# Optimization experiments

Measured on AMD Instinct MI355X. Metric: run time of the kernel, lower is better.

Reference implementation:

```python
import jax, jax.numpy as jnp
import numpy as np

B, T, C, H, HD = 4, 2048, 1024, 16, 64

def setup_inputs() -> dict:
    key = jax.random.key(0)
    ks = jax.random.split(key, 9)
    s = 1.0 / np.sqrt(C)
    return {
        "x":  jax.random.normal(ks[0], (B, T, C), jnp.float32),
        "Wq": jax.random.normal(ks[1], (H, C, HD), jnp.float32) * s,
        "bq": jax.random.normal(ks[2], (H, HD), jnp.float32) * 0.02,
        "Wk": jax.random.normal(ks[3], (H, C, HD), jnp.float32) * s,
        "bk": jax.random.normal(ks[4], (H, HD), jnp.float32) * 0.02,
        "Wv": jax.random.normal(ks[5], (H, C, HD), jnp.float32) * s,
        "bv": jax.random.normal(ks[6], (H, HD), jnp.float32) * 0.02,
        "Wo": jax.random.normal(ks[7], (C, C), jnp.float32) * s,
        "bo": jax.random.normal(ks[8], (C,), jnp.float32) * 0.02,
    }

def reference(x, Wq, bq, Wk, bk, Wv, bv, Wo, bo):
    # Batched per-head linear projections: [B,T,C] x [H,C,D] -> [B,H,T,D]
    q = jnp.einsum('btc,hcd->bhtd', x, Wq) + bq[None, :, None, :]
    k = jnp.einsum('btc,hcd->bhtd', x, Wk) + bk[None, :, None, :]
    v = jnp.einsum('btc,hcd->bhtd', x, Wv) + bv[None, :, None, :]
    scale = 1.0 / jnp.sqrt(jnp.asarray(HD, q.dtype))
    scores = jnp.einsum('bhtd,bhsd->bhts', q, k) * scale  # [B,H,T,T]
    causal = jnp.tril(jnp.ones((T, T), dtype=bool))
    scores = jnp.where(causal[None, None, :, :], scores, -jnp.inf)
    attn = jax.nn.softmax(scores, axis=-1)
    out = jnp.einsum('bhts,bhsd->bhtd', attn, v)          # [B,H,T,D]
    concat = out.transpose(0, 2, 1, 3).reshape(B, T, C)   # concat heads
    return concat @ Wo + bo
```

## Files before the change

### kernel.cpp

```cpp
#include <hip/hip_runtime.h>
#include <stdint.h>

#define TSEQ 2048
#define NHEAD 16

typedef __attribute__((ext_vector_type(8))) short bf16x8;
typedef __attribute__((ext_vector_type(4))) short bf16x4;
typedef __attribute__((ext_vector_type(4))) float f32x4;

__device__ __forceinline__ unsigned short f2bf(float f) {
  union { float f; uint32_t u; } c;
  c.f = f;
  uint32_t u = c.u;
  u += 0x7fffu + ((u >> 16) & 1u);
  return (unsigned short)(u >> 16);
}

__device__ __forceinline__ float fexp2(float x) {
#if __has_builtin(__builtin_amdgcn_exp2f)
  return __builtin_amdgcn_exp2f(x);
#else
  return __builtin_exp2f(x);
#endif
}

using as3_void  = __attribute__((address_space(3))) void;
using as1_cvoid = const __attribute__((address_space(1))) void;

__device__ __forceinline__ void gld_lds16(const void* g, void* l) {
  __builtin_amdgcn_global_load_lds((as1_cvoid*)g, (as3_void*)l, 16, 0, 0);
}


__global__ void prep_all(const float* __restrict__ x,
                         const float* __restrict__ Wq, const float* __restrict__ Wk,
                         const float* __restrict__ Wv, const float* __restrict__ Wo,
                         unsigned short* __restrict__ xb, unsigned short* __restrict__ BT,
                         unsigned short* __restrict__ WoT) {
  __shared__ unsigned short tile[64][72];
  const int bidx = blockIdx.x;
  const int t = threadIdx.x;
  if (bidx < 8192) {
    const int i = bidx * 256 + t;
    float4 v = ((const float4*)x)[i];
    int e = i * 4;
    int m = e >> 10, k = e & 1023;
    int ks = k ^ ((m & 7) << 3);
    ushort4 o;
    o.x = f2bf(v.x); o.y = f2bf(v.y); o.z = f2bf(v.z); o.w = f2bf(v.w);
    *(ushort4*)(xb + (size_t)m * 1024 + ks) = o;
  } else if (bidx < 8960) {
    const int bb = bidx - 8192;
    const int c0 = (bb & 15) * 64, h = (bb >> 4) & 15, z = bb >> 8;
    const float* W = (z == 0) ? Wq : (z == 1) ? Wk : Wv;
    const float* src = W + ((size_t)h * 1024 + c0) * 64;
#pragma unroll
    for (int p = 0; p < 16; ++p) {
      int idx = p * 256 + t;
      int cc = idx >> 6, d = idx & 63;
      tile[cc][d] = f2bf(src[(size_t)cc * 64 + d]);
    }
    __syncthreads();
    unsigned short* dst = BT + ((size_t)z * 1024 + (size_t)h * 64) * 1024 + c0;
#pragma unroll
    for (int p = 0; p < 16; ++p) {
      int idx = p * 256 + t;
      int d = idx >> 6, cc = idx & 63;
      dst[(size_t)d * 1024 + (cc ^ ((d & 7) << 3))] = tile[cc][d];
    }
  } else {
    const int bb = bidx - 8960;
    const int k0 = (bb & 15) * 64, n0 = (bb >> 4) * 64;
#pragma unroll
    for (int p = 0; p < 16; ++p) {
      int idx = p * 256 + t;
      int kk = idx >> 6, nn = idx & 63;
      tile[kk][nn] = f2bf(Wo[(size_t)(k0 + kk) * 1024 + n0 + nn]);
    }
    __syncthreads();
#pragma unroll
    for (int p = 0; p < 16; ++p) {
      int idx = p * 256 + t;
      int nn = idx >> 6, kk = idx & 63;
      WoT[(size_t)(n0 + nn) * 1024 + k0 + (kk ^ ((nn & 7) << 3))] = tile[kk][nn];
    }
  }
}


template <int MODE>
__global__ __launch_bounds__(256) void gemm_bt(
    const unsigned short* __restrict__ A, const unsigned short* __restrict__ BTm,
    const float* __restrict__ bias0, const float* __restrict__ bias1,
    const float* __restrict__ bias2,
    unsigned short* __restrict__ qo, unsigned short* __restrict__ ko,
    unsigned short* __restrict__ vto, float* __restrict__ outf,
    int K, int N) {
  __shared__ __align__(16) char lds[65536];

  const int tid = threadIdx.x, lane = tid & 63, wv = tid >> 6;
  const int wr = wv >> 1, wc = wv & 1;
  const int g = lane >> 4, r = lane & 15;
  const int m0 = blockIdx.x * 128, n0 = blockIdx.y * 128;
  const int xr = (r & 7) << 4;

  f32x4 acc[4][4] = {};

  const int arow = tid >> 3;
  const int acol = (tid & 7) * 8;
  const unsigned short* Ab = A + (size_t)(m0 + arow) * K + acol;
  const unsigned short* Bb = BTm + (size_t)(n0 + arow) * K + acol;

#define GSTAGE(b, kel) do {                                                 \
    char* ab_ = lds + (b) * 32768 + wv * 1024;                              \
    _Pragma("unroll") for (int i = 0; i < 4; ++i) {                         \
      gld_lds16(Ab + (size_t)i * 32 * K + (kel), ab_ + i * 4096);           \
      gld_lds16(Bb + (size_t)i * 32 * K + (kel), ab_ + 16384 + i * 4096);   \
    } } while (0)

  const int NT = K >> 6;
  GSTAGE(0, 0);
  __syncthreads();

  for (int t = 0; t < NT; ++t) {
    const int cur = t & 1;
    if (t + 1 < NT) GSTAGE(cur ^ 1, (t + 1) << 6);
    const char* Ar = lds + cur * 32768;
    const char* Br = Ar + 16384;
#pragma unroll
    for (int kk = 0; kk < 2; ++kk) {
      bf16x8 af[4], bfv[4];
#pragma unroll
      for (int f = 0; f < 4; ++f) {
        af[f]  = *(const bf16x8*)(Ar + (wr * 64 + f * 16 + r) * 128 + ((kk * 64 + g * 16) ^ xr));
        bfv[f] = *(const bf16x8*)(Br + (wc * 64 + f * 16 + r) * 128 + ((kk * 64 + g * 16) ^ xr));
      }
#pragma unroll
      for (int fm = 0; fm < 4; ++fm)
#pragma unroll
        for (int fn = 0; fn < 4; ++fn)
          acc[fm][fn] = __builtin_amdgcn_mfma_f32_16x16x32_bf16(af[fm], bfv[fn], acc[fm][fn], 0, 0, 0);
    }
    __syncthreads();
  }
#undef GSTAGE

  if (MODE == 0) {
    const int which = n0 >> 10;
    const float* bias = (which == 0) ? bias0 : (which == 1) ? bias1 : bias2;
    const float sc = (which == 0) ? 0.18033688011112042f : 1.0f;
    const int b = m0 >> 11;
    const int t0 = m0 & 2047;
    const int hb0 = (n0 & 1023) >> 6;
    unsigned short* ep = (unsigned short*)lds;

    __syncthreads();
    if (which == 2) {
#pragma unroll
      for (int fn = 0; fn < 4; ++fn) {
        const int dg = wc * 64 + fn * 16 + r;
        const float bvl = bias[(hb0 + (dg >> 6)) * 64 + (dg & 63)];
#pragma unroll
        for (int fm = 0; fm < 4; ++fm)
#pragma unroll
          for (int j = 0; j < 4; ++j) {
            const int t = wr * 64 + fm * 16 + 4 * g + j;
            ep[dg * 136 + t] = f2bf(acc[fm][fn][j] + bvl);
          }
      }
    } else {
#pragma unroll
      for (int fn = 0; fn < 4; ++fn) {
        const int dg = wc * 64 + fn * 16 + r;
        const float bvl = bias[(hb0 + (dg >> 6)) * 64 + (dg & 63)];
#pragma unroll
        for (int fm = 0; fm < 4; ++fm)
#pragma unroll
          for (int j = 0; j < 4; ++j) {
            const int t = wr * 64 + fm * 16 + 4 * g + j;
            ep[t * 136 + dg] = f2bf((acc[fm][fn][j] + bvl) * sc);
          }
      }
    }
    __syncthreads();
    if (which == 2) {
#pragma unroll
      for (int p = 0; p < 8; ++p) {
        const int idx = p * 256 + tid;
        const int dg = idx >> 4, u = idx & 15;
        const int head = hb0 + (dg >> 6), d = dg & 63;
        const size_t bhb = (size_t)(b * NHEAD + head) * 131072;
        const int c = u >> 3, w = u & 7;
        const int base_t = c * 64 + (w >> 2) * 32 + (w & 3) * 4;
        union { bf16x4 h4[2]; bf16x8 v8; } cc2;
        cc2.h4[0] = *(const bf16x4*)(ep + dg * 136 + base_t);
        cc2.h4[1] = *(const bf16x4*)(ep + dg * 136 + base_t + 16);
        *(bf16x8*)(vto + bhb + (size_t)((t0 >> 6) + c) * 4096 + (size_t)d * 64 +
                   ((w * 8) ^ ((d & 7) << 3))) = cc2.v8;
      }
    } else {
      unsigned short* qk = (which == 1) ? ko : qo;
#pragma unroll
      for (int p = 0; p < 8; ++p) {
        const int idx = p * 256 + tid;
        const int row = idx >> 4, seg = idx & 15;
        const int head = hb0 + (seg >> 3);
        const size_t bhb = (size_t)(b * NHEAD + head) * 131072;
        const bf16x8 v8 = *(const bf16x8*)(ep + row * 136 + seg * 8);
        const int tt = t0 + row;
        int dbase = (seg & 7) * 8;
        if (which == 1) dbase ^= (tt & 7) << 3;
        *(bf16x8*)(qk + bhb + (size_t)tt * 64 + dbase) = v8;
      }
    }
  } else {
    float* epf = (float*)lds;
#pragma unroll
    for (int h = 0; h < 2; ++h) {
      __syncthreads();
      if (wc == h) {
#pragma unroll
        for (int fn = 0; fn < 4; ++fn) {
          const int n = n0 + h * 64 + fn * 16 + r;
          const float bvl = bias0[n];
#pragma unroll
          for (int fm = 0; fm < 4; ++fm)
#pragma unroll
            for (int j = 0; j < 4; ++j)
              epf[(wr * 64 + fm * 16 + 4 * g + j) * 68 + fn * 16 + r] = acc[fm][fn][j] + bvl;
        }
      }
      __syncthreads();
#pragma unroll
      for (int p = 0; p < 8; ++p) {
        const int row = p * 16 + (tid >> 4);
        const int seg = tid & 15;
        const f32x4 v4 = *(const f32x4*)(epf + row * 68 + seg * 4);
        *(f32x4*)(outf + (size_t)(m0 + row) * N + n0 + h * 64 + seg * 4) = v4;
      }
    }
  }
}


__global__ __launch_bounds__(256) void attn_fwd(const unsigned short* __restrict__ Qm,
                                                const unsigned short* __restrict__ Km,
                                                const unsigned short* __restrict__ Vtm,
                                                unsigned short* __restrict__ Om) {
  __shared__ __align__(16) unsigned short Ks[2][4096];
  __shared__ __align__(16) unsigned short Vs[2][4096];

  const int tid = threadIdx.x, lane = tid & 63, wv = tid >> 6;
  const int g = lane >> 4, r = lane & 15;
  const int bh = blockIdx.x & 63;
  const int qp = 15 - (blockIdx.x >> 6);
  const int nt = qp * 2 + 2;

  const unsigned short* Qp = Qm + (size_t)bh * 131072;
  const unsigned short* Kp = Km + (size_t)bh * 131072;
  const unsigned short* Vp = Vtm + (size_t)bh * 131072;

  const int qb[2] = {qp * 128 + wv * 16, qp * 128 + 64 + wv * 16};

  bf16x8 qf[2][2];
#pragma unroll
  for (int mi = 0; mi < 2; ++mi)
#pragma unroll
    for (int h2 = 0; h2 < 2; ++h2)
      qf[mi][h2] = *(const bf16x8*)(Qp + (size_t)(qb[mi] + r) * 64 + h2 * 32 + g * 8);

  f32x4 oacc[2][4] = {};
  f32x4 lacc[2] = {};
  const short oneb = (short)0x3F80;
  const bf16x8 vones = {oneb, oneb, oneb, oneb, oneb, oneb, oneb, oneb};

  const uint32_t sw = (uint32_t)((r & 7) << 4);
  const uint32_t ob = (uint32_t)(r * 128);
  const uint32_t c0 = ((uint32_t)(g * 16)) ^ sw;
  const uint32_t c1 = ((uint32_t)(64 + g * 16)) ^ sw;
  const char* const KsB = (const char*)Ks;
  const char* const VsB = (const char*)Vs;

#define ASTAGE(buf, c) do {                                                      \
    const unsigned short* kg_ = Kp + (size_t)(c) * 4096;                         \
    const unsigned short* vg_ = Vp + (size_t)(c) * 4096;                         \
    const int o0_ = wv * 1024;                                                   \
    gld_lds16(kg_ + (o0_ >> 1) + lane * 8, (char*)Ks[buf] + o0_);                \
    gld_lds16(vg_ + (o0_ >> 1) + lane * 8, (char*)Vs[buf] + o0_);                \
    gld_lds16(kg_ + ((o0_ + 4096) >> 1) + lane * 8, (char*)Ks[buf] + o0_ + 4096);\
    gld_lds16(vg_ + ((o0_ + 4096) >> 1) + lane * 8, (char*)Vs[buf] + o0_ + 4096);\
  } while (0)

  ASTAGE(0, 0);
  __syncthreads();

  for (int t = 0; t < nt; ++t) {
    const uint32_t bo = (uint32_t)((t & 1) << 13);
    if (t + 1 < nt) ASTAGE((t & 1) ^ 1, t + 1);

    const char* pk0 = KsB + bo + ob + c0;
    const char* pk1 = KsB + bo + ob + c1;
    const char* pv0 = VsB + bo + ob + c0;
    const char* pv1 = VsB + bo + ob + c1;
    bf16x8 kf[4][2], vf[4][2];
#pragma unroll
    for (int tt = 0; tt < 4; ++tt) {
      kf[tt][0] = *(const bf16x8*)(pk0 + tt * 2048);
      kf[tt][1] = *(const bf16x8*)(pk1 + tt * 2048);
      vf[tt][0] = *(const bf16x8*)(pv0 + tt * 2048);
      vf[tt][1] = *(const bf16x8*)(pv1 + tt * 2048);
    }

#pragma unroll
    for (int mi = 0; mi < 2; ++mi) {
      const int qbm = qb[mi];
      if (t * 64 > qbm + 15) continue;

      f32x4 sT[4];
      __builtin_amdgcn_s_setprio(1);
#pragma unroll
      for (int tt = 0; tt < 4; ++tt) {
        f32x4 a = {0.f, 0.f, 0.f, 0.f};
        a = __builtin_amdgcn_mfma_f32_16x16x32_bf16(kf[tt][0], qf[mi][0], a, 0, 0, 0);
        a = __builtin_amdgcn_mfma_f32_16x16x32_bf16(kf[tt][1], qf[mi][1], a, 0, 0, 0);
        sT[tt] = a;
      }
      __builtin_amdgcn_s_setprio(0);

      const int qg = qbm + r;
      if (t * 64 + 63 > qbm) {
#pragma unroll
        for (int tt = 0; tt < 4; ++tt)
#pragma unroll
          for (int j = 0; j < 4; ++j) {
            const int kv = t * 64 + tt * 16 + 4 * g + j;
            sT[tt][j] = (kv <= qg) ? sT[tt][j] : -__builtin_inff();
          }
      }

#pragma unroll
      for (int tt = 0; tt < 4; ++tt)
#pragma unroll
        for (int j = 0; j < 4; ++j)
          sT[tt][j] = fexp2(sT[tt][j]);

      union { uint32_t w[8]; bf16x8 v[2]; } pu;
#pragma unroll
      for (int tt = 0; tt < 4; ++tt) {
        asm("v_cvt_pk_bf16_f32 %0, %1, %2" : "=v"(pu.w[2 * tt])
            : "v"(sT[tt][0]), "v"(sT[tt][1]));
        asm("v_cvt_pk_bf16_f32 %0, %1, %2" : "=v"(pu.w[2 * tt + 1])
            : "v"(sT[tt][2]), "v"(sT[tt][3]));
      }

      __builtin_amdgcn_s_setprio(1);
#pragma unroll
      for (int kk = 0; kk < 2; ++kk) {
#pragma unroll
        for (int df = 0; df < 4; ++df)
          oacc[mi][df] = __builtin_amdgcn_mfma_f32_16x16x32_bf16(pu.v[kk], vf[df][kk], oacc[mi][df], 0, 0, 0);
        lacc[mi] = __builtin_amdgcn_mfma_f32_16x16x32_bf16(pu.v[kk], vones, lacc[mi], 0, 0, 0);
      }
      __builtin_amdgcn_s_setprio(0);
    }
    __syncthreads();
  }
#undef ASTAGE

  const int b = bh >> 4, h = bh & 15;
#pragma unroll
  for (int mi = 0; mi < 2; ++mi) {
    float inv[4];
#pragma unroll
    for (int j = 0; j < 4; ++j) inv[j] = __builtin_amdgcn_rcpf(lacc[mi][j]);
#pragma unroll
    for (int df = 0; df < 4; ++df)
#pragma unroll
      for (int j = 0; j < 4; ++j) {
        const int trow = qb[mi] + 4 * g + j;
        const float ov = oacc[mi][df][j] * inv[j];
        const int col = (df * 16 + r) ^ ((trow & 7) << 3);
        Om[((size_t)(b * TSEQ + trow)) * 1024 + h * 64 + col] = f2bf(ov);
      }
  }
}


extern "C" void kernel_launch(void* const* d_in, const int* in_sizes, int n_in,
                              void* d_out, int out_size, void* d_ws, size_t ws_size,
                              hipStream_t stream) {
  const float* x  = (const float*)d_in[0];
  const float* Wq = (const float*)d_in[1];
  const float* bq = (const float*)d_in[2];
  const float* Wk = (const float*)d_in[3];
  const float* bk = (const float*)d_in[4];
  const float* Wv = (const float*)d_in[5];
  const float* bv = (const float*)d_in[6];
  const float* Wo = (const float*)d_in[7];
  const float* bo = (const float*)d_in[8];
  float* out = (float*)d_out;

  unsigned short* xb  = (unsigned short*)d_ws;
  unsigned short* btq = xb + (size_t)8192 * 1024;
  unsigned short* wot = btq + (size_t)3072 * 1024;
  unsigned short* qb  = wot + (size_t)1024 * 1024;
  unsigned short* kb  = qb + (size_t)64 * 2048 * 64;
  unsigned short* vtb = kb + (size_t)64 * 2048 * 64;

  prep_all<<<9216, 256, 0, stream>>>(x, Wq, Wk, Wv, Wo, xb, btq, wot);

  gemm_bt<0><<<dim3(64, 24), 256, 0, stream>>>(xb, btq, bq, bk, bv, qb, kb, vtb,
                                               nullptr, 1024, 3072);
  attn_fwd<<<1024, 256, 0, stream>>>(qb, kb, vtb, xb);
  gemm_bt<1><<<dim3(64, 8), 256, 0, stream>>>(xb, wot, bo, nullptr, nullptr,
                                              nullptr, nullptr, nullptr, out,
                                              1024, 1024);
}
```

Baseline: 164.3 us.

## Load K/V fragments directly from global memory instead of staging through LDS

The attention kernel drops its double-buffered LDS staging of K and V tiles (async global-to-LDS loads plus a block barrier each iteration). Each wave now reads its MFMA fragments straight from global memory. The XOR swizzle applied when the projection epilogue writes K and V^T is removed to match the new unswizzled read pattern. This removes the barriers and LDS traffic, but the four waves now each fetch the same K/V data from global memory or L2, and the loads are no longer prefetched one tile ahead.

```diff
diff --git a/kernel.cpp b/kernel.cpp
--- a/kernel.cpp
+++ b/kernel.cpp
@@ -196,7 +196,7 @@
         cc2.h4[0] = *(const bf16x4*)(ep + dg * 136 + base_t);
         cc2.h4[1] = *(const bf16x4*)(ep + dg * 136 + base_t + 16);
         *(bf16x8*)(vto + bhb + (size_t)((t0 >> 6) + c) * 4096 + (size_t)d * 64 +
-                   ((w * 8) ^ ((d & 7) << 3))) = cc2.v8;
+                   w * 8) = cc2.v8;
       }
     } else {
       unsigned short* qk = (which == 1) ? ko : qo;
@@ -208,9 +208,7 @@
         const size_t bhb = (size_t)(b * NHEAD + head) * 131072;
         const bf16x8 v8 = *(const bf16x8*)(ep + row * 136 + seg * 8);
         const int tt = t0 + row;
-        int dbase = (seg & 7) * 8;
-        if (which == 1) dbase ^= (tt & 7) << 3;
-        *(bf16x8*)(qk + bhb + (size_t)tt * 64 + dbase) = v8;
+        *(bf16x8*)(qk + bhb + (size_t)tt * 64 + (seg & 7) * 8) = v8;
       }
     }
   } else {
@@ -247,9 +245,6 @@
                                                 const unsigned short* __restrict__ Km,
                                                 const unsigned short* __restrict__ Vtm,
                                                 unsigned short* __restrict__ Om) {
-  __shared__ __align__(16) unsigned short Ks[2][4096];
-  __shared__ __align__(16) unsigned short Vs[2][4096];
-
   const int tid = threadIdx.x, lane = tid & 63, wv = tid >> 6;
   const int g = lane >> 4, r = lane & 15;
   const int bh = blockIdx.x & 63;
@@ -274,41 +269,18 @@
   const short oneb = (short)0x3F80;
   const bf16x8 vones = {oneb, oneb, oneb, oneb, oneb, oneb, oneb, oneb};
 
-  const uint32_t sw = (uint32_t)((r & 7) << 4);
-  const uint32_t ob = (uint32_t)(r * 128);
-  const uint32_t c0 = ((uint32_t)(g * 16)) ^ sw;
-  const uint32_t c1 = ((uint32_t)(64 + g * 16)) ^ sw;
-  const char* const KsB = (const char*)Ks;
-  const char* const VsB = (const char*)Vs;
-
-#define ASTAGE(buf, c) do {                                                      \
-    const unsigned short* kg_ = Kp + (size_t)(c) * 4096;                         \
-    const unsigned short* vg_ = Vp + (size_t)(c) * 4096;                         \
-    const int o0_ = wv * 1024;                                                   \
-    gld_lds16(kg_ + (o0_ >> 1) + lane * 8, (char*)Ks[buf] + o0_);                \
-    gld_lds16(vg_ + (o0_ >> 1) + lane * 8, (char*)Vs[buf] + o0_);                \
-    gld_lds16(kg_ + ((o0_ + 4096) >> 1) + lane * 8, (char*)Ks[buf] + o0_ + 4096);\
-    gld_lds16(vg_ + ((o0_ + 4096) >> 1) + lane * 8, (char*)Vs[buf] + o0_ + 4096);\
-  } while (0)
-
-  ASTAGE(0, 0);
-  __syncthreads();
+  const int fo = r * 64 + g * 8;
 
   for (int t = 0; t < nt; ++t) {
-    const uint32_t bo = (uint32_t)((t & 1) << 13);
-    if (t + 1 < nt) ASTAGE((t & 1) ^ 1, t + 1);
-
-    const char* pk0 = KsB + bo + ob + c0;
-    const char* pk1 = KsB + bo + ob + c1;
-    const char* pv0 = VsB + bo + ob + c0;
-    const char* pv1 = VsB + bo + ob + c1;
+    const unsigned short* Kt = Kp + (size_t)t * 4096 + fo;
+    const unsigned short* Vt = Vp + (size_t)t * 4096 + fo;
     bf16x8 kf[4][2], vf[4][2];
 #pragma unroll
     for (int tt = 0; tt < 4; ++tt) {
-      kf[tt][0] = *(const bf16x8*)(pk0 + tt * 2048);
-      kf[tt][1] = *(const bf16x8*)(pk1 + tt * 2048);
-      vf[tt][0] = *(const bf16x8*)(pv0 + tt * 2048);
-      vf[tt][1] = *(const bf16x8*)(pv1 + tt * 2048);
+      kf[tt][0] = *(const bf16x8*)(Kt + tt * 1024);
+      kf[tt][1] = *(const bf16x8*)(Kt + tt * 1024 + 32);
+      vf[tt][0] = *(const bf16x8*)(Vt + tt * 1024);
+      vf[tt][1] = *(const bf16x8*)(Vt + tt * 1024 + 32);
     }
 
 #pragma unroll
@@ -363,9 +335,7 @@
       }
       __builtin_amdgcn_s_setprio(0);
     }
-    __syncthreads();
-  }
-#undef ASTAGE
+  }
 
   const int b = bh >> 4, h = bh & 15;
 #pragma unroll
```

New measurement: 240.8 us. 1.47x slower.
